# Performance work log

Hardware: AMD Instinct MI355X
Metric: run time of the kernel (lower is better)

The kernel has to match this reference:

```python
import jax, jax.numpy as jnp
import numpy as np

D_MODEL = 1024
D_INNER = 2 * D_MODEL        # mambapy default expand=2
D_STATE = 16                 # mambapy default
D_CONV = 4                   # mambapy default
DT_RANK = D_MODEL // 16      # ceil(1024/16) = 64
D_FF = 4 * D_MODEL
BATCH = 2
SEQ = 2048


def setup_inputs() -> dict:
    key = jax.random.key(0)
    ks = jax.random.split(key, 12)
    s = 0.02
    rn = lambda k, shape: jax.random.normal(k, shape, jnp.float32) * s
    inp = {
        'x': jax.random.normal(ks[0], (BATCH, SEQ, D_MODEL), jnp.float32),
        'ln1_w': jnp.ones((D_MODEL,), jnp.float32),
        'ln1_b': jnp.zeros((D_MODEL,), jnp.float32),
        'in_proj_w': rn(ks[1], (2 * D_INNER, D_MODEL)),
        'conv_w': rn(ks[2], (D_INNER, 1, D_CONV)),
        'conv_b': jnp.zeros((D_INNER,), jnp.float32),
        'x_proj_w': rn(ks[3], (DT_RANK + 2 * D_STATE, D_INNER)),
        'dt_w': rn(ks[4], (D_INNER, DT_RANK)),
        'dt_b': jax.random.normal(ks[5], (D_INNER,), jnp.float32) * 0.5 - 4.0,
        'A_log': jnp.log(jnp.broadcast_to(jnp.arange(1, D_STATE + 1, dtype=jnp.float32), (D_INNER, D_STATE))),
        'Dskip': jnp.ones((D_INNER,), jnp.float32),
        'out_proj_w': rn(ks[6], (D_MODEL, D_INNER)),
        'ln2_w': jnp.ones((D_MODEL,), jnp.float32),
        'ln2_b': jnp.zeros((D_MODEL,), jnp.float32),
        'ff1_w': rn(ks[7], (D_FF, D_MODEL)),
        'ff1_b': jnp.zeros((D_FF,), jnp.float32),
        'ff2_w': rn(ks[8], (D_MODEL, D_FF)),
        'ff2_b': jnp.zeros((D_MODEL,), jnp.float32),
    }
    return inp


def _layernorm(x, w, b, eps=1e-5):
    m = jnp.mean(x, -1, keepdims=True)
    v = jnp.var(x, -1, keepdims=True)
    return (x - m) * jax.lax.rsqrt(v + eps) * w + b


def _mamba(y, in_proj_w, conv_w, conv_b, x_proj_w, dt_w, dt_b, A_log, Dskip, out_proj_w):
    # y: [B, L, d_model]
    xz = y @ in_proj_w.T                       # [B, L, 2*d_inner]
    xc, z = jnp.split(xz, 2, axis=-1)
    # causal depthwise conv1d over seq
    xt = xc.transpose(0, 2, 1)                 # [B, d_inner, L]
    xt = jax.lax.conv_general_dilated(
        xt, conv_w, (1,), [(D_CONV - 1, 0)],
        dimension_numbers=('NCH', 'OIH', 'NCH'),
        feature_group_count=D_INNER) + conv_b[None, :, None]
    u = jax.nn.silu(xt.transpose(0, 2, 1))     # [B, L, d_inner]
    dbc = u @ x_proj_w.T                       # [B, L, dt_rank + 2*d_state]
    dlt = jax.nn.softplus(dbc[..., :DT_RANK] @ dt_w.T + dt_b)   # [B, L, d_inner]
    Bm = dbc[..., DT_RANK:DT_RANK + D_STATE]   # [B, L, d_state]
    Cm = dbc[..., DT_RANK + D_STATE:]          # [B, L, d_state]
    A = -jnp.exp(A_log)                        # [d_inner, d_state]

    def step(h, inp):
        d, Bt, Ct, ut = inp                    # [B,d_inner],[B,d_state],[B,d_state],[B,d_inner]
        h = jnp.exp(d[:, :, None] * A) * h + (d * ut)[:, :, None] * Bt[:, None, :]
        yt = jnp.einsum('bds,bs->bd', h, Ct)
        return h, yt

    h0 = jnp.zeros((y.shape[0], D_INNER, D_STATE), y.dtype)
    xs = (dlt.transpose(1, 0, 2), Bm.transpose(1, 0, 2), Cm.transpose(1, 0, 2), u.transpose(1, 0, 2))
    _, ys = jax.lax.scan(step, h0, xs)         # ys: [L, B, d_inner]
    ysc = ys.transpose(1, 0, 2) + u * Dskip
    return (ysc * jax.nn.silu(z)) @ out_proj_w.T


def reference(x, ln1_w, ln1_b, in_proj_w, conv_w, conv_b, x_proj_w, dt_w, dt_b,
              A_log, Dskip, out_proj_w, ln2_w, ln2_b, ff1_w, ff1_b, ff2_w, ff2_b):
    y = _layernorm(x, ln1_w, ln1_b)
    y = _mamba(y, in_proj_w, conv_w, conv_b, x_proj_w, dt_w, dt_b, A_log, Dskip, out_proj_w)
    y = _layernorm(y, ln2_w, ln2_b)
    h = jax.nn.gelu(y @ ff1_w.T + ff1_b, approximate=False)
    y = h @ ff2_w.T + ff2_b
    return x + y
```

## Files before the change

### kernel.cpp

```cpp
#include <hip/hip_runtime.h>

#define DEV __device__ __forceinline__

typedef float f32x4 __attribute__((ext_vector_type(4)));
typedef short bf16x8 __attribute__((ext_vector_type(8)));

DEV unsigned short f2bf(float f) {
  union { float f; unsigned int u; } v; v.f = f;
  unsigned int r = v.u + 0x7FFFu + ((v.u >> 16) & 1u);
  return (unsigned short)(r >> 16);
}
DEV float bf2f(unsigned short h) {
  union { unsigned int u; float f; } v; v.u = ((unsigned int)h) << 16;
  return v.f;
}

DEV float fexp2(float x) {
#if defined(__has_builtin)
#if __has_builtin(__builtin_amdgcn_exp2f)
  return __builtin_amdgcn_exp2f(x);
#else
  float r; asm("v_exp_f32 %0, %1" : "=v"(r) : "v"(x)); return r;
#endif
#else
  float r; asm("v_exp_f32 %0, %1" : "=v"(r) : "v"(x)); return r;
#endif
}

DEV void gload16(const void* g, void* l) {
  __builtin_amdgcn_global_load_lds((const __attribute__((address_space(1))) void*)g,
                                   (__attribute__((address_space(3))) void*)l, 16, 0, 0);
}

template <int EPI>
__global__ __launch_bounds__(256) void gemm_bt(
    const unsigned short* __restrict__ A, const unsigned short* __restrict__ B,
    float* __restrict__ O1, float* __restrict__ O2, unsigned short* __restrict__ Ob,
    const float* __restrict__ bias, const float* __restrict__ resid,
    int M, int N, int K)
{
  __shared__ unsigned short As[128 * 64];
  __shared__ unsigned short Bs[128 * 64];
  const int tid = threadIdx.x;
  const int wave = tid >> 6;
  const int lane = tid & 63;
  const int brow = blockIdx.x * 128;
  const int bcol = blockIdx.y * 128;
  const int wr = (wave >> 1) * 64, wc = (wave & 1) * 64;
  const int lr = lane & 15, lq = lane >> 4;

  f32x4 acc[4][4];
#pragma unroll
  for (int m = 0; m < 4; ++m)
#pragma unroll
    for (int n = 0; n < 4; ++n)
#pragma unroll
      for (int j = 0; j < 4; ++j) acc[m][n][j] = 0.f;

  const size_t strideA = (size_t)K * 2;
  const char* Abase = (const char*)A + (size_t)brow * strideA;
  const char* Bbase = (const char*)B + (size_t)bcol * strideA;

  for (int k0 = 0; k0 < K; k0 += 64) {
#pragma unroll
    for (int is = 0; is < 4; ++is) {
      const int f = is * 4096 + tid * 16;
      const int row = f >> 7, colb = f & 127;
      char* la = (char*)As + is * 4096 + wave * 1024;
      char* lb = (char*)Bs + is * 4096 + wave * 1024;
      gload16(Abase + (size_t)row * strideA + (size_t)k0 * 2 + colb, la);
      gload16(Bbase + (size_t)row * strideA + (size_t)k0 * 2 + colb, lb);
    }
    asm volatile("s_waitcnt vmcnt(0)" ::: "memory");
    __syncthreads();
#pragma unroll
    for (int kk = 0; kk < 2; ++kk) {
      bf16x8 av[4], bv[4];
      const int ko = kk * 32 + lq * 8;
#pragma unroll
      for (int m = 0; m < 4; ++m)
        av[m] = *(const bf16x8*)&As[(wr + m * 16 + lr) * 64 + ko];
#pragma unroll
      for (int n = 0; n < 4; ++n)
        bv[n] = *(const bf16x8*)&Bs[(wc + n * 16 + lr) * 64 + ko];
#pragma unroll
      for (int m = 0; m < 4; ++m)
#pragma unroll
        for (int n = 0; n < 4; ++n)
          acc[m][n] = __builtin_amdgcn_mfma_f32_16x16x32_bf16(av[m], bv[n], acc[m][n], 0, 0, 0);
    }
    __syncthreads();
  }

#pragma unroll
  for (int m = 0; m < 4; ++m) {
#pragma unroll
    for (int n = 0; n < 4; ++n) {
      const int col = bcol + wc + n * 16 + lr;
      const int row0 = brow + wr + m * 16 + lq * 4;
#pragma unroll
      for (int j = 0; j < 4; ++j) {
        const int row = row0 + j;
        float v = acc[m][n][j];
        if (EPI == 0) {
          O1[(size_t)row * N + col] = v;
        } else if (EPI == 1) {
          v += bias[col];
          v = 0.5f * v * (1.f + erff(v * 0.70710678118654752f));
          Ob[(size_t)row * N + col] = f2bf(v);
        } else if (EPI == 2) {
          v += bias[col] + resid[(size_t)row * N + col];
          O1[(size_t)row * N + col] = v;
        } else if (EPI == 3) {
          v += bias[col];
          v = (v > 20.f) ? v : log1pf(expf(v));
          O1[(size_t)row * N + col] = v;
        } else {
          if (col < 2048) O1[(size_t)row * 2048 + col] = v;
          else O2[(size_t)row * 2048 + (col - 2048)] = v / (1.f + expf(-v));
        }
      }
    }
  }
}

__global__ __launch_bounds__(256) void ln_kernel(
    const float* __restrict__ x, const float* __restrict__ w,
    const float* __restrict__ b, unsigned short* __restrict__ out)
{
  const int row = blockIdx.x;
  const int tid = threadIdx.x;
  const float4 v = ((const float4*)(x + (size_t)row * 1024))[tid];
  float s = v.x + v.y + v.z + v.w;
  float sq = v.x * v.x + v.y * v.y + v.z * v.z + v.w * v.w;
#pragma unroll
  for (int m = 32; m >= 1; m >>= 1) { s += __shfl_xor(s, m); sq += __shfl_xor(sq, m); }
  __shared__ float ss[4], sqs[4];
  const int wave = tid >> 6;
  if ((tid & 63) == 0) { ss[wave] = s; sqs[wave] = sq; }
  __syncthreads();
  s = ss[0] + ss[1] + ss[2] + ss[3];
  sq = sqs[0] + sqs[1] + sqs[2] + sqs[3];
  const float mean = s * (1.f / 1024.f);
  const float var = sq * (1.f / 1024.f) - mean * mean;
  const float rstd = rsqrtf(var + 1e-5f);
  const float4 wv = ((const float4*)w)[tid];
  const float4 bv = ((const float4*)b)[tid];
  ushort4 o;
  o.x = f2bf((v.x - mean) * rstd * wv.x + bv.x);
  o.y = f2bf((v.y - mean) * rstd * wv.y + bv.y);
  o.z = f2bf((v.z - mean) * rstd * wv.z + bv.z);
  o.w = f2bf((v.w - mean) * rstd * wv.w + bv.w);
  ((ushort4*)(out + (size_t)row * 1024))[tid] = o;
}

__global__ __launch_bounds__(256) void conv_silu_kernel(
    const float* __restrict__ xc, const float* __restrict__ cw,
    const float* __restrict__ cb, unsigned short* __restrict__ u16)
{
  const int idx = blockIdx.x * 256 + threadIdx.x;
  const int d = idx & 2047;
  const int i = idx >> 11;
  const int t = i & 2047;
  float acc = cb[d];
#pragma unroll
  for (int k = 0; k < 4; ++k) {
    const int tt = t - 3 + k;
    if (tt >= 0) acc += xc[(size_t)(i - 3 + k) * 2048 + d] * cw[d * 4 + k];
  }
  const float s = acc / (1.f + expf(-acc));
  u16[idx] = f2bf(s);
}

__global__ __launch_bounds__(256) void cvt_weights(
    const float* __restrict__ w_in, unsigned short* __restrict__ d_in16,
    const float* __restrict__ w_ff1, unsigned short* __restrict__ d_ff1,
    const float* __restrict__ w_ff2, unsigned short* __restrict__ d_ff2,
    const float* __restrict__ w_out, unsigned short* __restrict__ d_out16,
    const float* __restrict__ w_dt, unsigned short* __restrict__ d_dt,
    const float* __restrict__ w_xp, unsigned short* __restrict__ d_xp)
{
  const int bid = blockIdx.x;
  const int tid = threadIdx.x;
  if (bid < 14336) {
    const float* s; unsigned short* d; int lb;
    if (bid < 4096)       { s = w_in;  d = d_in16;  lb = bid; }
    else if (bid < 8192)  { s = w_ff1; d = d_ff1;   lb = bid - 4096; }
    else if (bid < 12288) { s = w_ff2; d = d_ff2;   lb = bid - 8192; }
    else if (bid < 14336) { s = w_out; d = d_out16; lb = bid - 12288; }
    const int i = lb * 256 + tid;
    const float4 v = ((const float4*)s)[i];
    ((ushort4*)d)[i] = make_ushort4(f2bf(v.x), f2bf(v.y), f2bf(v.z), f2bf(v.w));
  } else if (bid < 14464) {
    const int i = (bid - 14336) * 256 + tid;
    const float4 v = ((const float4*)w_dt)[i];
    ((ushort4*)d_dt)[i] = make_ushort4(f2bf(v.x), f2bf(v.y), f2bf(v.z), f2bf(v.w));
  } else {
    const int i = (bid - 14464) * 256 + tid;
    const int r = (i * 4) >> 11;
    ushort4 o;
    if (r < 96) {
      const float4 v = ((const float4*)w_xp)[i];
      o = make_ushort4(f2bf(v.x), f2bf(v.y), f2bf(v.z), f2bf(v.w));
    } else {
      o = make_ushort4(0, 0, 0, 0);
    }
    ((ushort4*)d_xp)[i] = o;
  }
}

__global__ void cvt_adt_kernel(const float* __restrict__ dbc, unsigned short* __restrict__ adt) {
  const int idx = blockIdx.x * 256 + threadIdx.x;
  const int i = idx >> 6, r = idx & 63;
  adt[idx] = f2bf(dbc[(size_t)i * 128 + r]);
}

template <int NC>
__global__ __launch_bounds__(256) void scan_p1(
    const float* __restrict__ dlt, const unsigned short* __restrict__ u16,
    const float* __restrict__ dbc, const float* __restrict__ A_log,
    float* __restrict__ hpart, float* __restrict__ sdtp)
{
  constexpr int L = 2048 / NC;
  const int tid = threadIdx.x;
  const int c = blockIdx.x % NC;
  const int chg = blockIdx.x / NC;
  const int id = chg * 256 + tid;
  const int dch = id & 2047;
  const int b = id >> 11;
  float al2[16], h[16];
#pragma unroll
  for (int s = 0; s < 16; ++s) {
    al2[s] = -fexp2(A_log[dch * 16 + s] * 1.44269504f) * 1.44269504f;
    h[s] = 0.f;
  }
  const int i0 = b * 2048 + c * L;
  const int i0u = __builtin_amdgcn_readfirstlane(i0);
  const float* dptr = dlt + (size_t)i0 * 2048 + dch;
  const unsigned short* uptr = u16 + (size_t)i0 * 2048 + dch;
  const float* Bptr = dbc + (size_t)i0u * 128 + 64;
  float sdt = 0.f;
  for (int t = 0; t < L; ++t) {
    const float dt = *dptr;
    const float uu = bf2f(*uptr);
    const float dtu = dt * uu;
    const f32x4 B0 = *(const f32x4*)(Bptr + 0);
    const f32x4 B1 = *(const f32x4*)(Bptr + 4);
    const f32x4 B2 = *(const f32x4*)(Bptr + 8);
    const f32x4 B3 = *(const f32x4*)(Bptr + 12);
    sdt += dt;
#pragma unroll
    for (int s = 0; s < 16; ++s) {
      const float Bv = (s < 4) ? B0[s & 3] : (s < 8) ? B1[s & 3] : (s < 12) ? B2[s & 3] : B3[s & 3];
      h[s] = fexp2(dt * al2[s]) * h[s] + dtu * Bv;
    }
    dptr += 2048; uptr += 2048; Bptr += 128;
  }
  float* hp = hpart + ((size_t)(b * NC + c) * 2048 + dch) * 16;
#pragma unroll
  for (int s = 0; s < 16; ++s) hp[s] = h[s];
  sdtp[(size_t)(b * NC + c) * 2048 + dch] = sdt;
}

__global__ __launch_bounds__(256) void scan_prefix(
    const float* __restrict__ hpart, const float* __restrict__ sdtp,
    const float* __restrict__ A_log, float* __restrict__ hpre, int NC)
{
  const int g = blockIdx.x * 256 + threadIdx.x;
  const int s = g & 15;
  const int dch = (g >> 4) & 2047;
  const int b = g >> 15;
  const float al2 = -fexp2(A_log[dch * 16 + s] * 1.44269504f) * 1.44269504f;
  float run = 0.f;
  for (int c = 0; c < NC; ++c) {
    const size_t base = ((size_t)(b * NC + c) * 2048 + dch) * 16 + s;
    hpre[base] = run;
    run = fexp2(al2 * sdtp[(size_t)(b * NC + c) * 2048 + dch]) * run + hpart[base];
  }
}

template <int NC>
__global__ __launch_bounds__(256) void scan_p2(
    const float* __restrict__ dlt, const unsigned short* __restrict__ u16,
    const float* __restrict__ dbc, const float* __restrict__ zs,
    const float* __restrict__ A_log, const float* __restrict__ Dskip,
    const float* __restrict__ hpre, unsigned short* __restrict__ gated)
{
  constexpr int L = 2048 / NC;
  const int tid = threadIdx.x;
  const int c = blockIdx.x % NC;
  const int chg = blockIdx.x / NC;
  const int id = chg * 256 + tid;
  const int dch = id & 2047;
  const int b = id >> 11;
  float al2[16], h[16];
#pragma unroll
  for (int s = 0; s < 16; ++s)
    al2[s] = -fexp2(A_log[dch * 16 + s] * 1.44269504f) * 1.44269504f;
  const float* hb = hpre + ((size_t)(b * NC + c) * 2048 + dch) * 16;
#pragma unroll
  for (int s = 0; s < 16; ++s) h[s] = hb[s];
  const float Dsk = Dskip[dch];
  const int i0 = b * 2048 + c * L;
  const int i0u = __builtin_amdgcn_readfirstlane(i0);
  const float* dptr = dlt + (size_t)i0 * 2048 + dch;
  const unsigned short* uptr = u16 + (size_t)i0 * 2048 + dch;
  const float* zptr = zs + (size_t)i0 * 2048 + dch;
  const float* Bptr = dbc + (size_t)i0u * 128 + 64;
  unsigned short* gptr = gated + (size_t)i0 * 2048 + dch;
  for (int t = 0; t < L; ++t) {
    const float dt = *dptr;
    const float uu = bf2f(*uptr);
    const float zz = *zptr;
    const float dtu = dt * uu;
    const f32x4 B0 = *(const f32x4*)(Bptr + 0);
    const f32x4 B1 = *(const f32x4*)(Bptr + 4);
    const f32x4 B2 = *(const f32x4*)(Bptr + 8);
    const f32x4 B3 = *(const f32x4*)(Bptr + 12);
    const f32x4 C0 = *(const f32x4*)(Bptr + 16);
    const f32x4 C1 = *(const f32x4*)(Bptr + 20);
    const f32x4 C2 = *(const f32x4*)(Bptr + 24);
    const f32x4 C3 = *(const f32x4*)(Bptr + 28);
    float y0 = 0.f, y1 = 0.f, y2 = 0.f, y3 = 0.f;
#pragma unroll
    for (int s = 0; s < 16; ++s) {
      const float Bv = (s < 4) ? B0[s & 3] : (s < 8) ? B1[s & 3] : (s < 12) ? B2[s & 3] : B3[s & 3];
      const float Cv = (s < 4) ? C0[s & 3] : (s < 8) ? C1[s & 3] : (s < 12) ? C2[s & 3] : C3[s & 3];
      h[s] = fexp2(dt * al2[s]) * h[s] + dtu * Bv;
      if ((s & 3) == 0) y0 += h[s] * Cv;
      else if ((s & 3) == 1) y1 += h[s] * Cv;
      else if ((s & 3) == 2) y2 += h[s] * Cv;
      else y3 += h[s] * Cv;
    }
    const float y = (y0 + y1) + (y2 + y3);
    *gptr = f2bf((y + uu * Dsk) * zz);
    dptr += 2048; uptr += 2048; zptr += 2048; Bptr += 128; gptr += 2048;
  }
}

extern "C" void kernel_launch(void* const* d_in, const int* in_sizes, int n_in,
                              void* d_out, int out_size, void* d_ws, size_t ws_size,
                              hipStream_t stream) {
  const float* x         = (const float*)d_in[0];
  const float* ln1_w     = (const float*)d_in[1];
  const float* ln1_b     = (const float*)d_in[2];
  const float* in_proj_w = (const float*)d_in[3];
  const float* conv_w    = (const float*)d_in[4];
  const float* conv_b    = (const float*)d_in[5];
  const float* x_proj_w  = (const float*)d_in[6];
  const float* dt_w      = (const float*)d_in[7];
  const float* dt_b      = (const float*)d_in[8];
  const float* A_log     = (const float*)d_in[9];
  const float* Dskip     = (const float*)d_in[10];
  const float* out_proj_w= (const float*)d_in[11];
  const float* ln2_w     = (const float*)d_in[12];
  const float* ln2_b     = (const float*)d_in[13];
  const float* ff1_w     = (const float*)d_in[14];
  const float* ff1_b     = (const float*)d_in[15];
  const float* ff2_w     = (const float*)d_in[16];
  const float* ff2_b     = (const float*)d_in[17];
  float* out = (float*)d_out;

  char* ws = (char*)d_ws;
  size_t off = 0;
  auto alloc = [&](size_t bytes) {
    char* p = ws + off;
    off += (bytes + 255) & ~(size_t)255;
    return p;
  };
  unsigned short* w16_in  = (unsigned short*)alloc(4096ull * 1024 * 2);
  unsigned short* w16_xp  = (unsigned short*)alloc(128ull * 2048 * 2);
  unsigned short* w16_dt  = (unsigned short*)alloc(2048ull * 64 * 2);
  unsigned short* w16_out = (unsigned short*)alloc(1024ull * 2048 * 2);
  unsigned short* w16_ff1 = (unsigned short*)alloc(4096ull * 1024 * 2);
  unsigned short* w16_ff2 = (unsigned short*)alloc(1024ull * 4096 * 2);
  unsigned short* y16     = (unsigned short*)alloc(4096ull * 1024 * 2);
  float* xcbuf            = (float*)alloc(4096ull * 2048 * 4);
  unsigned short* u16     = (unsigned short*)alloc(4096ull * 2048 * 2);
  float* slotA            = (float*)alloc(2048ull * 4096 * 4);
  float* zs               = (float*)alloc(2048ull * 4096 * 4);
  float* dbc              = (float*)alloc(4096ull * 128 * 4);
  unsigned short* adt16   = (unsigned short*)alloc(4096ull * 64 * 2);
  float* dlt              = (float*)alloc(2048ull * 4096 * 4);
  (void)ws_size; (void)in_sizes; (void)n_in; (void)out_size;

  constexpr int NC = 128;
  float* c2 = xcbuf;
  unsigned short* t2_16 = (unsigned short*)((char*)xcbuf + 4096ull * 1024 * 4);
  float* hpart = slotA;
  unsigned short* gated16 = (unsigned short*)slotA;
  unsigned short* h16 = (unsigned short*)slotA;
  float* hpre  = xcbuf;
  float* sdtp  = (float*)y16;

  cvt_weights<<<14720, 256, 0, stream>>>(in_proj_w, w16_in, ff1_w, w16_ff1,
                                         ff2_w, w16_ff2, out_proj_w, w16_out,
                                         dt_w, w16_dt, x_proj_w, w16_xp);

  ln_kernel<<<4096, 256, 0, stream>>>(x, ln1_w, ln1_b, y16);
  gemm_bt<5><<<dim3(32, 32), 256, 0, stream>>>(y16, w16_in, xcbuf, zs, nullptr, nullptr, nullptr, 4096, 4096, 1024);
  conv_silu_kernel<<<32768, 256, 0, stream>>>(xcbuf, conv_w, conv_b, u16);
  gemm_bt<0><<<dim3(32, 1), 256, 0, stream>>>(u16, w16_xp, dbc, nullptr, nullptr, nullptr, nullptr, 4096, 128, 2048);
  cvt_adt_kernel<<<1024, 256, 0, stream>>>(dbc, adt16);
  gemm_bt<3><<<dim3(32, 16), 256, 0, stream>>>(adt16, w16_dt, dlt, nullptr, nullptr, dt_b, nullptr, 4096, 2048, 64);
  scan_p1<NC><<<16 * NC, 256, 0, stream>>>(dlt, u16, dbc, A_log, hpart, sdtp);
  scan_prefix<<<256, 256, 0, stream>>>(hpart, sdtp, A_log, hpre, NC);
  scan_p2<NC><<<16 * NC, 256, 0, stream>>>(dlt, u16, dbc, zs, A_log, Dskip, hpre, gated16);
  gemm_bt<0><<<dim3(32, 8), 256, 0, stream>>>(gated16, w16_out, c2, nullptr, nullptr, nullptr, nullptr, 4096, 1024, 2048);
  ln_kernel<<<4096, 256, 0, stream>>>(c2, ln2_w, ln2_b, t2_16);
  gemm_bt<1><<<dim3(32, 32), 256, 0, stream>>>(t2_16, w16_ff1, nullptr, nullptr, h16, ff1_b, nullptr, 4096, 4096, 1024);
  gemm_bt<2><<<dim3(32, 8), 256, 0, stream>>>(h16, w16_ff2, out, nullptr, nullptr, ff2_b, x, 4096, 1024, 4096);
}
```

Measured before the change: 626.6 us.

## Store intermediates in bf16, split-K x_proj GEMM, and smaller N tiles for narrow GEMMs

The in_proj GEMM now writes xc and silu(z) as bf16, and the dt GEMM writes delta as bf16, which reduces the bytes read by the conv and scan kernels. The x_proj GEMM, which previously launched only 32 blocks, is split along K into 8 slices with a reduction kernel that also produces the bf16 dt-rank input, replacing the separate convert kernel. The GEMM template gains BM/BN parameters, and the N=1024 GEMMs use 128x64 tiles to double the block count. The cost is a small loss of precision in delta and z, plus an extra partial-sum buffer.

Result: faster. 588.8 us (-6.0%).

```diff
diff --git a/kernel.cpp b/kernel.cpp
--- a/kernel.cpp
+++ b/kernel.cpp
@@ -32,70 +32,75 @@
                                    (__attribute__((address_space(3))) void*)l, 16, 0, 0);
 }
 
-template <int EPI>
+template <int BM, int BN, int EPI>
 __global__ __launch_bounds__(256) void gemm_bt(
     const unsigned short* __restrict__ A, const unsigned short* __restrict__ B,
-    float* __restrict__ O1, float* __restrict__ O2, unsigned short* __restrict__ Ob,
+    float* __restrict__ O1, unsigned short* __restrict__ Ob, unsigned short* __restrict__ Ob2,
     const float* __restrict__ bias, const float* __restrict__ resid,
-    int M, int N, int K)
-{
-  __shared__ unsigned short As[128 * 64];
-  __shared__ unsigned short Bs[128 * 64];
+    int M, int N, int K, int Kstride)
+{
+  constexpr int MR = BM / 32, NR = BN / 32;
+  __shared__ unsigned short As[BM * 64];
+  __shared__ unsigned short Bs[BN * 64];
   const int tid = threadIdx.x;
   const int wave = tid >> 6;
   const int lane = tid & 63;
-  const int brow = blockIdx.x * 128;
-  const int bcol = blockIdx.y * 128;
-  const int wr = (wave >> 1) * 64, wc = (wave & 1) * 64;
+  const int brow = blockIdx.x * BM;
+  const int bcol = blockIdx.y * BN;
+  const int koff = blockIdx.z * K;
+  const int wr = (wave >> 1) * (BM / 2), wc = (wave & 1) * (BN / 2);
   const int lr = lane & 15, lq = lane >> 4;
 
-  f32x4 acc[4][4];
-#pragma unroll
-  for (int m = 0; m < 4; ++m)
-#pragma unroll
-    for (int n = 0; n < 4; ++n)
+  f32x4 acc[MR][NR];
+#pragma unroll
+  for (int m = 0; m < MR; ++m)
+#pragma unroll
+    for (int n = 0; n < NR; ++n)
 #pragma unroll
       for (int j = 0; j < 4; ++j) acc[m][n][j] = 0.f;
 
-  const size_t strideA = (size_t)K * 2;
-  const char* Abase = (const char*)A + (size_t)brow * strideA;
-  const char* Bbase = (const char*)B + (size_t)bcol * strideA;
+  const size_t strideA = (size_t)Kstride * 2;
+  const char* Abase = (const char*)A + (size_t)brow * strideA + (size_t)koff * 2;
+  const char* Bbase = (const char*)B + (size_t)bcol * strideA + (size_t)koff * 2;
+  const int srow = tid >> 3;
+  const int scol = (tid & 7) * 16;
 
   for (int k0 = 0; k0 < K; k0 += 64) {
 #pragma unroll
-    for (int is = 0; is < 4; ++is) {
-      const int f = is * 4096 + tid * 16;
-      const int row = f >> 7, colb = f & 127;
+    for (int is = 0; is < MR; ++is) {
       char* la = (char*)As + is * 4096 + wave * 1024;
+      gload16(Abase + (size_t)(is * 32 + srow) * strideA + (size_t)k0 * 2 + scol, la);
+    }
+#pragma unroll
+    for (int is = 0; is < NR; ++is) {
       char* lb = (char*)Bs + is * 4096 + wave * 1024;
-      gload16(Abase + (size_t)row * strideA + (size_t)k0 * 2 + colb, la);
-      gload16(Bbase + (size_t)row * strideA + (size_t)k0 * 2 + colb, lb);
+      gload16(Bbase + (size_t)(is * 32 + srow) * strideA + (size_t)k0 * 2 + scol, lb);
     }
     asm volatile("s_waitcnt vmcnt(0)" ::: "memory");
     __syncthreads();
 #pragma unroll
     for (int kk = 0; kk < 2; ++kk) {
-      bf16x8 av[4], bv[4];
+      bf16x8 av[MR], bv[NR];
       const int ko = kk * 32 + lq * 8;
 #pragma unroll
-      for (int m = 0; m < 4; ++m)
+      for (int m = 0; m < MR; ++m)
         av[m] = *(const bf16x8*)&As[(wr + m * 16 + lr) * 64 + ko];
 #pragma unroll
-      for (int n = 0; n < 4; ++n)
+      for (int n = 0; n < NR; ++n)
         bv[n] = *(const bf16x8*)&Bs[(wc + n * 16 + lr) * 64 + ko];
 #pragma unroll
-      for (int m = 0; m < 4; ++m)
-#pragma unroll
-        for (int n = 0; n < 4; ++n)
+      for (int m = 0; m < MR; ++m)
+#pragma unroll
+        for (int n = 0; n < NR; ++n)
           acc[m][n] = __builtin_amdgcn_mfma_f32_16x16x32_bf16(av[m], bv[n], acc[m][n], 0, 0, 0);
     }
     __syncthreads();
   }
 
 #pragma unroll
-  for (int m = 0; m < 4; ++m) {
-#pragma unroll
-    for (int n = 0; n < 4; ++n) {
+  for (int m = 0; m < MR; ++m) {
+#pragma unroll
+    for (int n = 0; n < NR; ++n) {
       const int col = bcol + wc + n * 16 + lr;
       const int row0 = brow + wr + m * 16 + lq * 4;
 #pragma unroll
@@ -114,14 +119,29 @@
         } else if (EPI == 3) {
           v += bias[col];
           v = (v > 20.f) ? v : log1pf(expf(v));
-          O1[(size_t)row * N + col] = v;
+          Ob[(size_t)row * N + col] = f2bf(v);
+        } else if (EPI == 5) {
+          if (col < 2048) Ob[(size_t)row * 2048 + col] = f2bf(v);
+          else Ob2[(size_t)row * 2048 + (col - 2048)] = f2bf(v / (1.f + expf(-v)));
         } else {
-          if (col < 2048) O1[(size_t)row * 2048 + col] = v;
-          else O2[(size_t)row * 2048 + (col - 2048)] = v / (1.f + expf(-v));
+          O1[((size_t)blockIdx.z * M + row) * N + col] = v;
         }
       }
     }
   }
+}
+
+__global__ __launch_bounds__(256) void xproj_reduce(
+    const float* __restrict__ pbuf, float* __restrict__ dbc,
+    unsigned short* __restrict__ adt)
+{
+  const int idx = blockIdx.x * 256 + threadIdx.x;
+  float s = 0.f;
+#pragma unroll
+  for (int z = 0; z < 8; ++z) s += pbuf[(size_t)z * 524288 + idx];
+  dbc[idx] = s;
+  const int r = idx & 127;
+  if (r < 64) adt[(size_t)(idx >> 7) * 64 + r] = f2bf(s);
 }
 
 __global__ __launch_bounds__(256) void ln_kernel(
@@ -155,7 +175,7 @@
 }
 
 __global__ __launch_bounds__(256) void conv_silu_kernel(
-    const float* __restrict__ xc, const float* __restrict__ cw,
+    const unsigned short* __restrict__ xc16, const float* __restrict__ cw,
     const float* __restrict__ cb, unsigned short* __restrict__ u16)
 {
   const int idx = blockIdx.x * 256 + threadIdx.x;
@@ -166,7 +186,7 @@
 #pragma unroll
   for (int k = 0; k < 4; ++k) {
     const int tt = t - 3 + k;
-    if (tt >= 0) acc += xc[(size_t)(i - 3 + k) * 2048 + d] * cw[d * 4 + k];
+    if (tt >= 0) acc += bf2f(xc16[(size_t)(i - 3 + k) * 2048 + d]) * cw[d * 4 + k];
   }
   const float s = acc / (1.f + expf(-acc));
   u16[idx] = f2bf(s);
@@ -187,7 +207,7 @@
     if (bid < 4096)       { s = w_in;  d = d_in16;  lb = bid; }
     else if (bid < 8192)  { s = w_ff1; d = d_ff1;   lb = bid - 4096; }
     else if (bid < 12288) { s = w_ff2; d = d_ff2;   lb = bid - 8192; }
-    else if (bid < 14336) { s = w_out; d = d_out16; lb = bid - 12288; }
+    else                  { s = w_out; d = d_out16; lb = bid - 12288; }
     const int i = lb * 256 + tid;
     const float4 v = ((const float4*)s)[i];
     ((ushort4*)d)[i] = make_ushort4(f2bf(v.x), f2bf(v.y), f2bf(v.z), f2bf(v.w));
@@ -209,15 +229,9 @@
   }
 }
 
-__global__ void cvt_adt_kernel(const float* __restrict__ dbc, unsigned short* __restrict__ adt) {
-  const int idx = blockIdx.x * 256 + threadIdx.x;
-  const int i = idx >> 6, r = idx & 63;
-  adt[idx] = f2bf(dbc[(size_t)i * 128 + r]);
-}
-
 template <int NC>
 __global__ __launch_bounds__(256) void scan_p1(
-    const float* __restrict__ dlt, const unsigned short* __restrict__ u16,
+    const unsigned short* __restrict__ dlt, const unsigned short* __restrict__ u16,
     const float* __restrict__ dbc, const float* __restrict__ A_log,
     float* __restrict__ hpart, float* __restrict__ sdtp)
 {
@@ -236,12 +250,12 @@
   }
   const int i0 = b * 2048 + c * L;
   const int i0u = __builtin_amdgcn_readfirstlane(i0);
-  const float* dptr = dlt + (size_t)i0 * 2048 + dch;
+  const unsigned short* dptr = dlt + (size_t)i0 * 2048 + dch;
   const unsigned short* uptr = u16 + (size_t)i0 * 2048 + dch;
   const float* Bptr = dbc + (size_t)i0u * 128 + 64;
   float sdt = 0.f;
   for (int t = 0; t < L; ++t) {
-    const float dt = *dptr;
+    const float dt = bf2f(*dptr);
     const float uu = bf2f(*uptr);
     const float dtu = dt * uu;
     const f32x4 B0 = *(const f32x4*)(Bptr + 0);
@@ -281,8 +295,8 @@
 
 template <int NC>
 __global__ __launch_bounds__(256) void scan_p2(
-    const float* __restrict__ dlt, const unsigned short* __restrict__ u16,
-    const float* __restrict__ dbc, const float* __restrict__ zs,
+    const unsigned short* __restrict__ dlt, const unsigned short* __restrict__ u16,
+    const float* __restrict__ dbc, const unsigned short* __restrict__ zs16,
     const float* __restrict__ A_log, const float* __restrict__ Dskip,
     const float* __restrict__ hpre, unsigned short* __restrict__ gated)
 {
@@ -303,15 +317,15 @@
   const float Dsk = Dskip[dch];
   const int i0 = b * 2048 + c * L;
   const int i0u = __builtin_amdgcn_readfirstlane(i0);
-  const float* dptr = dlt + (size_t)i0 * 2048 + dch;
+  const unsigned short* dptr = dlt + (size_t)i0 * 2048 + dch;
   const unsigned short* uptr = u16 + (size_t)i0 * 2048 + dch;
-  const float* zptr = zs + (size_t)i0 * 2048 + dch;
+  const unsigned short* zptr = zs16 + (size_t)i0 * 2048 + dch;
   const float* Bptr = dbc + (size_t)i0u * 128 + 64;
   unsigned short* gptr = gated + (size_t)i0 * 2048 + dch;
   for (int t = 0; t < L; ++t) {
-    const float dt = *dptr;
+    const float dt = bf2f(*dptr);
     const float uu = bf2f(*uptr);
-    const float zz = *zptr;
+    const float zz = bf2f(*zptr);
     const float dtu = dt * uu;
     const f32x4 B0 = *(const f32x4*)(Bptr + 0);
     const f32x4 B1 = *(const f32x4*)(Bptr + 4);
@@ -375,22 +389,25 @@
   unsigned short* w16_ff1 = (unsigned short*)alloc(4096ull * 1024 * 2);
   unsigned short* w16_ff2 = (unsigned short*)alloc(1024ull * 4096 * 2);
   unsigned short* y16     = (unsigned short*)alloc(4096ull * 1024 * 2);
-  float* xcbuf            = (float*)alloc(4096ull * 2048 * 4);
+  char* slotX             = alloc(4096ull * 2048 * 4);
   unsigned short* u16     = (unsigned short*)alloc(4096ull * 2048 * 2);
-  float* slotA            = (float*)alloc(2048ull * 4096 * 4);
-  float* zs               = (float*)alloc(2048ull * 4096 * 4);
+  char* slotA             = alloc(2048ull * 4096 * 4);
+  unsigned short* zs16    = (unsigned short*)alloc(4096ull * 2048 * 2);
   float* dbc              = (float*)alloc(4096ull * 128 * 4);
   unsigned short* adt16   = (unsigned short*)alloc(4096ull * 64 * 2);
-  float* dlt              = (float*)alloc(2048ull * 4096 * 4);
+  char* slotD             = alloc(2048ull * 4096 * 4);
   (void)ws_size; (void)in_sizes; (void)n_in; (void)out_size;
 
   constexpr int NC = 128;
-  float* c2 = xcbuf;
-  unsigned short* t2_16 = (unsigned short*)((char*)xcbuf + 4096ull * 1024 * 4);
-  float* hpart = slotA;
+  unsigned short* xc16 = (unsigned short*)slotX;
+  float* hpre  = (float*)slotX;
+  float* c2 = (float*)slotX;
+  unsigned short* t2_16 = (unsigned short*)(slotX + 4096ull * 1024 * 4);
+  float* hpart = (float*)slotA;
   unsigned short* gated16 = (unsigned short*)slotA;
   unsigned short* h16 = (unsigned short*)slotA;
-  float* hpre  = xcbuf;
+  float* pbuf  = (float*)slotD;
+  unsigned short* dlt16 = (unsigned short*)slotD;
   float* sdtp  = (float*)y16;
 
   cvt_weights<<<14720, 256, 0, stream>>>(in_proj_w, w16_in, ff1_w, w16_ff1,
@@ -398,16 +415,16 @@
                                          dt_w, w16_dt, x_proj_w, w16_xp);
 
   ln_kernel<<<4096, 256, 0, stream>>>(x, ln1_w, ln1_b, y16);
-  gemm_bt<5><<<dim3(32, 32), 256, 0, stream>>>(y16, w16_in, xcbuf, zs, nullptr, nullptr, nullptr, 4096, 4096, 1024);
-  conv_silu_kernel<<<32768, 256, 0, stream>>>(xcbuf, conv_w, conv_b, u16);
-  gemm_bt<0><<<dim3(32, 1), 256, 0, stream>>>(u16, w16_xp, dbc, nullptr, nullptr, nullptr, nullptr, 4096, 128, 2048);
-  cvt_adt_kernel<<<1024, 256, 0, stream>>>(dbc, adt16);
-  gemm_bt<3><<<dim3(32, 16), 256, 0, stream>>>(adt16, w16_dt, dlt, nullptr, nullptr, dt_b, nullptr, 4096, 2048, 64);
-  scan_p1<NC><<<16 * NC, 256, 0, stream>>>(dlt, u16, dbc, A_log, hpart, sdtp);
+  gemm_bt<128, 128, 5><<<dim3(32, 32), 256, 0, stream>>>(y16, w16_in, nullptr, xc16, zs16, nullptr, nullptr, 4096, 4096, 1024, 1024);
+  conv_silu_kernel<<<32768, 256, 0, stream>>>(xc16, conv_w, conv_b, u16);
+  gemm_bt<128, 128, 6><<<dim3(32, 1, 8), 256, 0, stream>>>(u16, w16_xp, pbuf, nullptr, nullptr, nullptr, nullptr, 4096, 128, 256, 2048);
+  xproj_reduce<<<2048, 256, 0, stream>>>(pbuf, dbc, adt16);
+  gemm_bt<128, 128, 3><<<dim3(32, 16), 256, 0, stream>>>(adt16, w16_dt, nullptr, dlt16, nullptr, dt_b, nullptr, 4096, 2048, 64, 64);
+  scan_p1<NC><<<16 * NC, 256, 0, stream>>>(dlt16, u16, dbc, A_log, hpart, sdtp);
   scan_prefix<<<256, 256, 0, stream>>>(hpart, sdtp, A_log, hpre, NC);
-  scan_p2<NC><<<16 * NC, 256, 0, stream>>>(dlt, u16, dbc, zs, A_log, Dskip, hpre, gated16);
-  gemm_bt<0><<<dim3(32, 8), 256, 0, stream>>>(gated16, w16_out, c2, nullptr, nullptr, nullptr, nullptr, 4096, 1024, 2048);
+  scan_p2<NC><<<16 * NC, 256, 0, stream>>>(dlt16, u16, dbc, zs16, A_log, Dskip, hpre, gated16);
+  gemm_bt<128, 64, 0><<<dim3(32, 16), 256, 0, stream>>>(gated16, w16_out, c2, nullptr, nullptr, nullptr, nullptr, 4096, 1024, 2048, 2048);
   ln_kernel<<<4096, 256, 0, stream>>>(c2, ln2_w, ln2_b, t2_16);
-  gemm_bt<1><<<dim3(32, 32), 256, 0, stream>>>(t2_16, w16_ff1, nullptr, nullptr, h16, ff1_b, nullptr, 4096, 4096, 1024);
-  gemm_bt<2><<<dim3(32, 8), 256, 0, stream>>>(h16, w16_ff2, out, nullptr, nullptr, ff2_b, x, 4096, 1024, 4096);
-}
+  gemm_bt<128, 128, 1><<<dim3(32, 32), 256, 0, stream>>>(t2_16, w16_ff1, nullptr, h16, nullptr, ff1_b, nullptr, 4096, 4096, 1024, 1024);
+  gemm_bt<128, 64, 2><<<dim3(32, 16), 256, 0, stream>>>(h16, w16_ff2, out, nullptr, nullptr, ff2_b, x, 4096, 1024, 4096, 4096);
+}
```
